# Kernel optimization log

Measured on AMD Instinct MI355X. Metric: run time of the kernel, lower is better.

Reference implementation:

```python
import jax, jax.numpy as jnp
import numpy as np

B, L, P, A = 32, 512, 128, 128   # batch, prot seq len, prot dim, atom dim
N = 1024                          # total atoms (32 per molecule)
H1, H2 = 512, 256                 # hidden_list


def setup_inputs() -> dict:
    key = jax.random.key(0)
    ks = jax.random.split(key, 12)
    atom_embed = jax.random.normal(ks[0], (N, A), dtype=jnp.float32)
    protSeq_embed = jax.random.normal(ks[1], (B, L, P), dtype=jnp.float32)
    # sorted segment ids, every segment non-empty (32 atoms per molecule)
    atom_splits = jnp.repeat(jnp.arange(B, dtype=jnp.int64), N // B)
    s = 0.05
    att1_W = jax.random.normal(ks[2], (P + A, 128), dtype=jnp.float32) * s
    att1_b = jnp.zeros((128,), dtype=jnp.float32)
    att2_W = jax.random.normal(ks[3], (128, 1), dtype=jnp.float32) * s
    att2_b = jnp.zeros((1,), dtype=jnp.float32)
    d1_W = jax.random.normal(ks[4], (A + P, H1), dtype=jnp.float32) * s
    d1_b = jnp.zeros((H1,), dtype=jnp.float32)
    d2_W = jax.random.normal(ks[5], (H1, H2), dtype=jnp.float32) * s
    d2_b = jnp.zeros((H2,), dtype=jnp.float32)
    out_W = jax.random.normal(ks[6], (H2, 1), dtype=jnp.float32) * s
    out_b = jnp.zeros((1,), dtype=jnp.float32)
    return {"atom_embed": atom_embed, "protSeq_embed": protSeq_embed,
            "atom_splits": atom_splits,
            "att1_W": att1_W, "att1_b": att1_b, "att2_W": att2_W, "att2_b": att2_b,
            "d1_W": d1_W, "d1_b": d1_b, "d2_W": d2_W, "d2_b": d2_b,
            "out_W": out_W, "out_b": out_b}


def reference(atom_embed, protSeq_embed, atom_splits,
              att1_W, att1_b, att2_W, att2_b,
              d1_W, d1_b, d2_W, d2_b, out_W, out_b):
    num_seg = protSeq_embed.shape[0]
    # gather protein rows per atom: [N, L, P]
    prot_g = protSeq_embed[atom_splits]
    # concat with broadcast atom embed: [N, L, P+A]
    atom_x = jnp.broadcast_to(atom_embed[:, None, :], prot_g.shape[:2] + atom_embed.shape[-1:])
    concat = jnp.concatenate([prot_g, atom_x], axis=-1)
    # attention MLP -> scores W: [N, L]
    hid = jnp.tanh(concat @ att1_W + att1_b)
    W = 5.0 * jnp.tanh(hid @ att2_W + att2_b)[..., 0]
    # atom-side weights: exp(max over seq), normalized per segment
    Wc = jnp.exp(jnp.max(W, axis=-1, keepdims=True))                     # [N, 1]
    Sc = jax.ops.segment_sum(Wc, atom_splits, num_segments=num_seg)[atom_splits]
    aa = Wc / Sc                                                          # [N, 1]
    atom_pool = jax.ops.segment_sum(aa * atom_embed, atom_splits, num_segments=num_seg)  # [B, A]
    # protein-side: segment-max scores, softmax over seq, weighted sum
    Wp = jax.ops.segment_max(W, atom_splits, num_segments=num_seg)       # [B, L]
    ap = jax.nn.softmax(Wp, axis=-1)
    prot_pool = jnp.einsum('bl,bld->bd', ap, protSeq_embed)              # [B, P]
    z = jnp.concatenate([atom_pool, prot_pool], axis=-1)
    z = jax.nn.relu(z @ d1_W + d1_b)
    z = jax.nn.relu(z @ d2_W + d2_b)
    return z @ out_W + out_b                                             # [B, 1]
```

## Files before the change

### kernel.cpp

```cpp
#include <hip/hip_runtime.h>
#include <math.h>

#define NATOMS 1024
#define BSEG   32
#define LSEQ   512

__device__ __forceinline__ float fast_tanh(float x) {
    x = fminf(fmaxf(x, -20.0f), 20.0f);
    float e = __expf(2.0f * x);
    return __fdividef(e - 1.0f, e + 1.0f);
}

__device__ __forceinline__ float trm(float c, float p, float e) {
    return c * __builtin_amdgcn_rcpf(fmaf(p, e, 1.0f));
}

__global__ __launch_bounds__(256) void gemm_exp_kernel(
    const float* __restrict__ protSeq, const float* __restrict__ atom_embed,
    const float* __restrict__ att1_W, const float* __restrict__ att1_b,
    float* __restrict__ ep, float* __restrict__ eb,
    float* __restrict__ zr, float* __restrict__ dp)
{
    __shared__ float xT[64 * 68];
    __shared__ float wsb[64 * 132];
    const int tid = threadIdx.x, bx = blockIdx.x;

    const float* Xb; const float* Wb; const float* bb; float* outp;
    if (bx < 256) {
        Xb = protSeq + (long)bx * 64 * 128; Wb = att1_W; bb = att1_b;
        outp = ep + (long)bx * 64 * 128;
    } else {
        int e = bx - 256;
        zr[e * 256 + tid] = 0.0f;
        if (e == 0 && tid < 32) dp[tid] = 0.0f;
        Xb = atom_embed + (long)e * 64 * 128; Wb = att1_W + 128 * 128; bb = nullptr;
        outp = eb + (long)e * 64 * 128;
    }
    const int tx = tid & 15, ty = tid >> 4;

    float acc[4][8];
    #pragma unroll
    for (int i = 0; i < 4; ++i)
        #pragma unroll
        for (int j = 0; j < 8; ++j) acc[i][j] = 0.0f;

    #pragma unroll
    for (int half = 0; half < 2; ++half) {
        if (half) __syncthreads();
        #pragma unroll
        for (int t = 0; t < 4; ++t) {
            int flat = (tid + 256 * t) * 4;
            int r = flat >> 6, kk = flat & 63;
            float4 v = *(const float4*)&Xb[r * 128 + half * 64 + kk];
            xT[kk * 68 + r] = v.x; xT[(kk + 1) * 68 + r] = v.y;
            xT[(kk + 2) * 68 + r] = v.z; xT[(kk + 3) * 68 + r] = v.w;
        }
        #pragma unroll
        for (int t = 0; t < 8; ++t) {
            int flat = (tid + 256 * t) * 4;
            int kk = flat >> 7, c = flat & 127;
            *(float4*)&wsb[kk * 132 + c] = *(const float4*)&Wb[(half * 64 + kk) * 128 + c];
        }
        __syncthreads();
        #pragma unroll 4
        for (int kk = 0; kk < 64; ++kk) {
            float4 a  = *(const float4*)&xT[kk * 68 + 4 * ty];
            float4 w0 = *(const float4*)&wsb[kk * 132 + 8 * tx];
            float4 w1 = *(const float4*)&wsb[kk * 132 + 8 * tx + 4];
            #pragma unroll
            for (int i = 0; i < 4; ++i) {
                float av = (i == 0) ? a.x : (i == 1) ? a.y : (i == 2) ? a.z : a.w;
                acc[i][0] += av * w0.x; acc[i][1] += av * w0.y;
                acc[i][2] += av * w0.z; acc[i][3] += av * w0.w;
                acc[i][4] += av * w1.x; acc[i][5] += av * w1.y;
                acc[i][6] += av * w1.z; acc[i][7] += av * w1.w;
            }
        }
    }
    float bias[8];
    #pragma unroll
    for (int j = 0; j < 8; ++j) bias[j] = 0.0f;
    if (bb) {
        *(float4*)&bias[0] = *(const float4*)&bb[8 * tx];
        *(float4*)&bias[4] = *(const float4*)&bb[8 * tx + 4];
    }
    #pragma unroll
    for (int i = 0; i < 4; ++i) {
        float o[8];
        #pragma unroll
        for (int j = 0; j < 8; ++j) {
            float v = fminf(fmaxf(acc[i][j] + bias[j], -20.0f), 20.0f);
            o[j] = __expf(2.0f * v);
        }
        int row = 4 * ty + i;
        *(float4*)&outp[row * 128 + 8 * tx]     = make_float4(o[0], o[1], o[2], o[3]);
        *(float4*)&outp[row * 128 + 8 * tx + 4] = make_float4(o[4], o[5], o[6], o[7]);
    }
}

__global__ __launch_bounds__(256) void score3_kernel(
    const float* __restrict__ ep, const float* __restrict__ eb,
    const float* __restrict__ att2_W, const float* __restrict__ att2_b,
    const float* __restrict__ protSeq,
    float* __restrict__ pmax, float* __restrict__ zr, float* __restrict__ dp)
{
    __shared__ float eps[64 * 132];
    __shared__ float ebs[32 * 132];
    __shared__ float c_s[128];
    __shared__ float wps[64];
    __shared__ float es[64];
    __shared__ float pmn[32 * 33];
    __shared__ float part[256];
    __shared__ float base_s;
    const int tid = threadIdx.x;
    const int chunk = blockIdx.x, b = blockIdx.y;
    const int lbase = chunk * 64;

    #pragma unroll
    for (int t = 0; t < 8; ++t) {
        int flat = (tid + 256 * t) * 4;
        int l = flat >> 7, j = flat & 127;
        *(float4*)&eps[l * 132 + j] =
            *(const float4*)&ep[((long)(b * 512 + lbase + l)) * 128 + j];
    }
    #pragma unroll
    for (int t = 0; t < 4; ++t) {
        int flat = (tid + 256 * t) * 4;
        int n = flat >> 7, j = flat & 127;
        *(float4*)&ebs[n * 132 + j] = *(const float4*)&eb[(b * 32 + n) * 128 + j];
    }
    if (tid < 128) c_s[tid] = -2.0f * att2_W[tid];
    __syncthreads();
    if (tid < 64) {
        float s = c_s[tid] + c_s[tid + 64];
        #pragma unroll
        for (int m = 1; m < 64; m <<= 1) s += __shfl_xor(s, m);
        if (tid == 0) base_s = -0.5f * s + att2_b[0];
    }
    __syncthreads();

    const int ng = tid & 7, lg = tid >> 3;
    const float* e0 = &ebs[ng * 132];
    const float* e1 = &ebs[(ng + 8) * 132];
    const float* e2 = &ebs[(ng + 16) * 132];
    const float* e3 = &ebs[(ng + 24) * 132];
    const float* p0 = &eps[lg * 132];
    const float* p1 = &eps[(lg + 32) * 132];
    float a00 = 0, a01 = 0, a10 = 0, a11 = 0, a20 = 0, a21 = 0, a30 = 0, a31 = 0;
    #pragma unroll 2
    for (int jj = 0; jj < 128; jj += 4) {
        float4 c4 = *(const float4*)&c_s[jj];
        float4 q0 = *(const float4*)(p0 + jj);
        float4 q1 = *(const float4*)(p1 + jj);
        float4 b0 = *(const float4*)(e0 + jj);
        float4 b1 = *(const float4*)(e1 + jj);
        float4 b2v = *(const float4*)(e2 + jj);
        float4 b3 = *(const float4*)(e3 + jj);
#define DOCOMP(C, Q0, Q1, B0, B1, B2, B3) \
        a00 += trm(C, Q0, B0); a01 += trm(C, Q1, B0); \
        a10 += trm(C, Q0, B1); a11 += trm(C, Q1, B1); \
        a20 += trm(C, Q0, B2); a21 += trm(C, Q1, B2); \
        a30 += trm(C, Q0, B3); a31 += trm(C, Q1, B3);
        DOCOMP(c4.x, q0.x, q1.x, b0.x, b1.x, b2v.x, b3.x)
        DOCOMP(c4.y, q0.y, q1.y, b0.y, b1.y, b2v.y, b3.y)
        DOCOMP(c4.z, q0.z, q1.z, b0.z, b1.z, b2v.z, b3.z)
        DOCOMP(c4.w, q0.w, q1.w, b0.w, b1.w, b2v.w, b3.w)
#undef DOCOMP
    }
    const float bs = base_s;
    float W00 = 5.0f * fast_tanh(a00 + bs), W01 = 5.0f * fast_tanh(a01 + bs);
    float W10 = 5.0f * fast_tanh(a10 + bs), W11 = 5.0f * fast_tanh(a11 + bs);
    float W20 = 5.0f * fast_tanh(a20 + bs), W21 = 5.0f * fast_tanh(a21 + bs);
    float W30 = 5.0f * fast_tanh(a30 + bs), W31 = 5.0f * fast_tanh(a31 + bs);

    float m0 = fmaxf(fmaxf(W00, W10), fmaxf(W20, W30));
    float m1 = fmaxf(fmaxf(W01, W11), fmaxf(W21, W31));
    #pragma unroll
    for (int d = 1; d < 8; d <<= 1) {
        m0 = fmaxf(m0, __shfl_xor(m0, d));
        m1 = fmaxf(m1, __shfl_xor(m1, d));
    }
    if (ng == 0) { wps[lg] = m0; wps[lg + 32] = m1; }
    pmn[lg * 33 + ng]      = fmaxf(W00, W01);
    pmn[lg * 33 + ng + 8]  = fmaxf(W10, W11);
    pmn[lg * 33 + ng + 16] = fmaxf(W20, W21);
    pmn[lg * 33 + ng + 24] = fmaxf(W30, W31);
    __syncthreads();
    if (tid < 32) {
        float m = pmn[tid];
        #pragma unroll
        for (int g = 1; g < 32; ++g) m = fmaxf(m, pmn[g * 33 + tid]);
        pmax[b * 256 + chunk * 32 + tid] = m;
    }
    if (tid < 64) es[tid] = __expf(wps[tid]);
    __syncthreads();
    if (tid < 64) {
        float v = es[tid];
        #pragma unroll
        for (int d = 1; d < 64; d <<= 1) v += __shfl_xor(v, d);
        if (tid == 0) atomicAdd(&dp[b], v);
    }
    const int dd = tid & 127, hf = tid >> 7;
    float az = 0.0f;
    #pragma unroll 4
    for (int i = 0; i < 32; ++i)
        az += es[hf * 32 + i] *
              protSeq[((long)(b * 512 + lbase + hf * 32 + i)) * 128 + dd];
    part[tid] = az;
    __syncthreads();
    if (tid < 128) atomicAdd(&zr[b * 128 + tid], part[tid] + part[128 + tid]);
}

__global__ __launch_bounds__(256) void mlp1_kernel(
    const float* __restrict__ pmax, const float* __restrict__ atom_embed,
    const float* __restrict__ zr, const float* __restrict__ dp,
    const float* __restrict__ d1_W, const float* __restrict__ d1_b,
    const float* __restrict__ out_b, float* __restrict__ h1,
    float* __restrict__ out)
{
    __shared__ float zs[256];
    __shared__ float part[4 * 65];
    __shared__ float expw[32];
    __shared__ float sinv_s;
    const int tid = threadIdx.x;
    const int cx = blockIdx.x, b = blockIdx.y;
    if (tid < 32) {
        float m = -1e30f;
        #pragma unroll
        for (int c = 0; c < 8; ++c) m = fmaxf(m, pmax[b * 256 + c * 32 + tid]);
        float e = __expf(m);
        expw[tid] = e;
        #pragma unroll
        for (int d = 1; d < 32; d <<= 1) e += __shfl_xor(e, d);
        if (tid == 0) sinv_s = 1.0f / e;
    }
    if (cx == 0 && tid == 0) out[b] = out_b[0];
    __syncthreads();
    if (tid < 128) {
        float a = 0.0f;
        #pragma unroll 4
        for (int n = 0; n < 32; ++n)
            a += expw[n] * atom_embed[(b * 32 + n) * 128 + tid];
        zs[tid] = a * sinv_s;
    } else {
        zs[tid] = zr[b * 128 + tid - 128] * (1.0f / dp[b]);
    }
    __syncthreads();
    const int c0 = cx * 64, ci = tid & 63, kg = tid >> 6;
    float acc = 0.0f;
    #pragma unroll 8
    for (int k = kg * 64; k < kg * 64 + 64; ++k)
        acc += zs[k] * d1_W[k * 512 + c0 + ci];
    part[kg * 65 + ci] = acc;
    __syncthreads();
    if (tid < 64) {
        float s = part[tid] + part[65 + tid] + part[130 + tid] + part[195 + tid]
                + d1_b[c0 + tid];
        h1[b * 512 + c0 + tid] = fmaxf(s, 0.0f);
    }
}

__global__ __launch_bounds__(256) void mlp2_kernel(
    const float* __restrict__ h1, const float* __restrict__ d2_W,
    const float* __restrict__ d2_b, const float* __restrict__ out_W,
    float* __restrict__ out)
{
    __shared__ float hs[512];
    __shared__ float part[8 * 33];
    const int tid = threadIdx.x;
    const int c0 = blockIdx.x * 32, b = blockIdx.y;
    hs[tid] = h1[b * 512 + tid];
    hs[tid + 256] = h1[b * 512 + 256 + tid];
    __syncthreads();
    const int ci = tid & 31, kg = tid >> 5;
    float acc = 0.0f;
    #pragma unroll 8
    for (int k = kg * 64; k < kg * 64 + 64; ++k)
        acc += hs[k] * d2_W[k * 256 + c0 + ci];
    part[kg * 33 + ci] = acc;
    __syncthreads();
    if (tid < 32) {
        float s = d2_b[c0 + tid];
        #pragma unroll
        for (int g = 0; g < 8; ++g) s += part[g * 33 + tid];
        float contrib = fmaxf(s, 0.0f) * out_W[c0 + tid];
        #pragma unroll
        for (int m = 16; m; m >>= 1) contrib += __shfl_xor(contrib, m);
        if (tid == 0) atomicAdd(&out[b], contrib);
    }
}

extern "C" void kernel_launch(void* const* d_in, const int* in_sizes, int n_in,
                              void* d_out, int out_size, void* d_ws, size_t ws_size,
                              hipStream_t stream) {
    const float* atom_embed = (const float*)d_in[0];
    const float* protSeq    = (const float*)d_in[1];
    const float* att1_W = (const float*)d_in[3];
    const float* att1_b = (const float*)d_in[4];
    const float* att2_W = (const float*)d_in[5];
    const float* att2_b = (const float*)d_in[6];
    const float* d1_W   = (const float*)d_in[7];
    const float* d1_b   = (const float*)d_in[8];
    const float* d2_W   = (const float*)d_in[9];
    const float* d2_b   = (const float*)d_in[10];
    const float* out_W  = (const float*)d_in[11];
    const float* out_b  = (const float*)d_in[12];
    float* out = (float*)d_out;

    float* ws = (float*)d_ws;
    float* ep   = ws;
    float* eb   = ep + 2097152;
    float* pmax = eb + 131072;
    float* zr   = pmax + 8192;
    float* dp   = zr + 4096;
    float* h1   = dp + 32;

    gemm_exp_kernel<<<272, 256, 0, stream>>>(protSeq, atom_embed, att1_W,
                                             att1_b, ep, eb, zr, dp);
    score3_kernel<<<dim3(8, BSEG), 256, 0, stream>>>(ep, eb, att2_W, att2_b,
                                                     protSeq, pmax, zr, dp);
    mlp1_kernel<<<dim3(8, BSEG), 256, 0, stream>>>(pmax, atom_embed, zr, dp,
                                                   d1_W, d1_b, out_b, h1, out);
    mlp2_kernel<<<dim3(8, BSEG), 256, 0, stream>>>(h1, d2_W, d2_b, out_W, out);
}
```

Measured before the change: 127.1 us.

## Fuse all stages into one cooperative kernel with grid syncs

Replaces the four kernel launches with a single cooperative kernel of 256 blocks that uses grid-wide syncs between phases. The att1 projection of the protein chunk is kept in shared memory and consumed directly by the scoring stage, so the 8 MB exp-projection intermediate no longer round-trips through global memory. The per-atom projection is spread across the chunk blocks, and the final MLP runs in one block per batch. This removes launch gaps and global traffic, but adds grid-sync cost and leaves 7 of 8 blocks idle during the serial MLP tail.

```diff
diff --git a/kernel.cpp b/kernel.cpp
--- a/kernel.cpp
+++ b/kernel.cpp
@@ -1,5 +1,8 @@
 #include <hip/hip_runtime.h>
+#include <hip/hip_cooperative_groups.h>
 #include <math.h>
+
+namespace cg = cooperative_groups;
 
 #define NATOMS 1024
 #define BSEG   32
@@ -10,283 +13,282 @@
     float e = __expf(2.0f * x);
     return __fdividef(e - 1.0f, e + 1.0f);
 }
-
 __device__ __forceinline__ float trm(float c, float p, float e) {
     return c * __builtin_amdgcn_rcpf(fmaf(p, e, 1.0f));
 }
 
-__global__ __launch_bounds__(256) void gemm_exp_kernel(
-    const float* __restrict__ protSeq, const float* __restrict__ atom_embed,
+#define EPS_SZ  8448
+#define REG2_SZ 13312
+
+__global__ void __launch_bounds__(256) mega_kernel(
+    const float* __restrict__ atom_embed, const float* __restrict__ protSeq,
     const float* __restrict__ att1_W, const float* __restrict__ att1_b,
-    float* __restrict__ ep, float* __restrict__ eb,
-    float* __restrict__ zr, float* __restrict__ dp)
+    const float* __restrict__ att2_W, const float* __restrict__ att2_b,
+    const float* __restrict__ d1_W, const float* __restrict__ d1_b,
+    const float* __restrict__ d2_W, const float* __restrict__ d2_b,
+    const float* __restrict__ out_W, const float* __restrict__ out_b,
+    float* __restrict__ eb, float* __restrict__ pmax,
+    float* __restrict__ zr, float* __restrict__ dp, float* __restrict__ out)
 {
-    __shared__ float xT[64 * 68];
-    __shared__ float wsb[64 * 132];
-    const int tid = threadIdx.x, bx = blockIdx.x;
-
-    const float* Xb; const float* Wb; const float* bb; float* outp;
-    if (bx < 256) {
-        Xb = protSeq + (long)bx * 64 * 128; Wb = att1_W; bb = att1_b;
-        outp = ep + (long)bx * 64 * 128;
-    } else {
-        int e = bx - 256;
-        zr[e * 256 + tid] = 0.0f;
-        if (e == 0 && tid < 32) dp[tid] = 0.0f;
-        Xb = atom_embed + (long)e * 64 * 128; Wb = att1_W + 128 * 128; bb = nullptr;
-        outp = eb + (long)e * 64 * 128;
-    }
-    const int tx = tid & 15, ty = tid >> 4;
-
-    float acc[4][8];
-    #pragma unroll
-    for (int i = 0; i < 4; ++i)
-        #pragma unroll
-        for (int j = 0; j < 8; ++j) acc[i][j] = 0.0f;
-
-    #pragma unroll
-    for (int half = 0; half < 2; ++half) {
-        if (half) __syncthreads();
-        #pragma unroll
-        for (int t = 0; t < 4; ++t) {
-            int flat = (tid + 256 * t) * 4;
-            int r = flat >> 6, kk = flat & 63;
-            float4 v = *(const float4*)&Xb[r * 128 + half * 64 + kk];
-            xT[kk * 68 + r] = v.x; xT[(kk + 1) * 68 + r] = v.y;
-            xT[(kk + 2) * 68 + r] = v.z; xT[(kk + 3) * 68 + r] = v.w;
-        }
-        #pragma unroll
-        for (int t = 0; t < 8; ++t) {
-            int flat = (tid + 256 * t) * 4;
-            int kk = flat >> 7, c = flat & 127;
-            *(float4*)&wsb[kk * 132 + c] = *(const float4*)&Wb[(half * 64 + kk) * 128 + c];
-        }
-        __syncthreads();
-        #pragma unroll 4
-        for (int kk = 0; kk < 64; ++kk) {
-            float4 a  = *(const float4*)&xT[kk * 68 + 4 * ty];
-            float4 w0 = *(const float4*)&wsb[kk * 132 + 8 * tx];
-            float4 w1 = *(const float4*)&wsb[kk * 132 + 8 * tx + 4];
-            #pragma unroll
-            for (int i = 0; i < 4; ++i) {
-                float av = (i == 0) ? a.x : (i == 1) ? a.y : (i == 2) ? a.z : a.w;
-                acc[i][0] += av * w0.x; acc[i][1] += av * w0.y;
-                acc[i][2] += av * w0.z; acc[i][3] += av * w0.w;
-                acc[i][4] += av * w1.x; acc[i][5] += av * w1.y;
-                acc[i][6] += av * w1.z; acc[i][7] += av * w1.w;
-            }
-        }
-    }
-    float bias[8];
-    #pragma unroll
-    for (int j = 0; j < 8; ++j) bias[j] = 0.0f;
-    if (bb) {
-        *(float4*)&bias[0] = *(const float4*)&bb[8 * tx];
-        *(float4*)&bias[4] = *(const float4*)&bb[8 * tx + 4];
-    }
-    #pragma unroll
-    for (int i = 0; i < 4; ++i) {
-        float o[8];
-        #pragma unroll
-        for (int j = 0; j < 8; ++j) {
-            float v = fminf(fmaxf(acc[i][j] + bias[j], -20.0f), 20.0f);
-            o[j] = __expf(2.0f * v);
-        }
-        int row = 4 * ty + i;
-        *(float4*)&outp[row * 128 + 8 * tx]     = make_float4(o[0], o[1], o[2], o[3]);
-        *(float4*)&outp[row * 128 + 8 * tx + 4] = make_float4(o[4], o[5], o[6], o[7]);
-    }
-}
-
-__global__ __launch_bounds__(256) void score3_kernel(
-    const float* __restrict__ ep, const float* __restrict__ eb,
-    const float* __restrict__ att2_W, const float* __restrict__ att2_b,
-    const float* __restrict__ protSeq,
-    float* __restrict__ pmax, float* __restrict__ zr, float* __restrict__ dp)
-{
-    __shared__ float eps[64 * 132];
-    __shared__ float ebs[32 * 132];
-    __shared__ float c_s[128];
-    __shared__ float wps[64];
-    __shared__ float es[64];
-    __shared__ float pmn[32 * 33];
-    __shared__ float part[256];
-    __shared__ float base_s;
+    __shared__ float smem[EPS_SZ + REG2_SZ];
+    float* eps  = smem;
+    float* reg2 = smem + EPS_SZ;
     const int tid = threadIdx.x;
     const int chunk = blockIdx.x, b = blockIdx.y;
     const int lbase = chunk * 64;
 
-    #pragma unroll
-    for (int t = 0; t < 8; ++t) {
-        int flat = (tid + 256 * t) * 4;
-        int l = flat >> 7, j = flat & 127;
-        *(float4*)&eps[l * 132 + j] =
-            *(const float4*)&ep[((long)(b * 512 + lbase + l)) * 128 + j];
+    {
+        float* xT  = reg2;
+        float* wsb = reg2 + 4352;
+        float* xTa = reg2 + 12800;
+
+        if (chunk == 2 && tid < 128) zr[b * 128 + tid] = 0.0f;
+        if (chunk == 1 && tid == 0) dp[b] = 0.0f;
+
+        for (int i = tid; i < 128; i += 256) {
+            int r = i >> 5, c = i & 31;
+            float4 v = *(const float4*)&atom_embed[(b * 32 + chunk * 4 + r) * 128 + 4 * c];
+            xTa[(4 * c + 0) * 4 + r] = v.x;
+            xTa[(4 * c + 1) * 4 + r] = v.y;
+            xTa[(4 * c + 2) * 4 + r] = v.z;
+            xTa[(4 * c + 3) * 4 + r] = v.w;
+        }
+
+        const int tx = tid & 15, ty = tid >> 4;
+        const float* Xb = protSeq + ((long)(b * 512 + lbase)) * 128;
+        float acc[4][8];
+        #pragma unroll
+        for (int i = 0; i < 4; ++i)
+            #pragma unroll
+            for (int j = 0; j < 8; ++j) acc[i][j] = 0.0f;
+
+        #pragma unroll
+        for (int half = 0; half < 2; ++half) {
+            if (half) __syncthreads();
+            #pragma unroll
+            for (int t = 0; t < 4; ++t) {
+                int flat = (tid + 256 * t) * 4;
+                int r = flat >> 6, kk = flat & 63;
+                float4 v = *(const float4*)&Xb[r * 128 + half * 64 + kk];
+                xT[kk * 68 + r] = v.x; xT[(kk + 1) * 68 + r] = v.y;
+                xT[(kk + 2) * 68 + r] = v.z; xT[(kk + 3) * 68 + r] = v.w;
+            }
+            #pragma unroll
+            for (int t = 0; t < 8; ++t) {
+                int flat = (tid + 256 * t) * 4;
+                int kk = flat >> 7, c = flat & 127;
+                *(float4*)&wsb[kk * 132 + c] =
+                    *(const float4*)&att1_W[(half * 64 + kk) * 128 + c];
+            }
+            __syncthreads();
+            #pragma unroll 4
+            for (int kk = 0; kk < 64; ++kk) {
+                float4 a  = *(const float4*)&xT[kk * 68 + 4 * ty];
+                float4 w0 = *(const float4*)&wsb[kk * 132 + 8 * tx];
+                float4 w1 = *(const float4*)&wsb[kk * 132 + 8 * tx + 4];
+                #pragma unroll
+                for (int i = 0; i < 4; ++i) {
+                    float av = (i == 0) ? a.x : (i == 1) ? a.y : (i == 2) ? a.z : a.w;
+                    acc[i][0] += av * w0.x; acc[i][1] += av * w0.y;
+                    acc[i][2] += av * w0.z; acc[i][3] += av * w0.w;
+                    acc[i][4] += av * w1.x; acc[i][5] += av * w1.y;
+                    acc[i][6] += av * w1.z; acc[i][7] += av * w1.w;
+                }
+            }
+        }
+        float bias[8];
+        *(float4*)&bias[0] = *(const float4*)&att1_b[8 * tx];
+        *(float4*)&bias[4] = *(const float4*)&att1_b[8 * tx + 4];
+        #pragma unroll
+        for (int i = 0; i < 4; ++i) {
+            float o[8];
+            #pragma unroll
+            for (int j = 0; j < 8; ++j) {
+                float v = fminf(fmaxf(acc[i][j] + bias[j], -20.0f), 20.0f);
+                o[j] = __expf(2.0f * v);
+            }
+            int row = 4 * ty + i;
+            *(float4*)&eps[row * 132 + 8 * tx]     = make_float4(o[0], o[1], o[2], o[3]);
+            *(float4*)&eps[row * 132 + 8 * tx + 4] = make_float4(o[4], o[5], o[6], o[7]);
+        }
+        if (tid < 32) {
+            float a2[4][4];
+            #pragma unroll
+            for (int i = 0; i < 4; ++i)
+                #pragma unroll
+                for (int j = 0; j < 4; ++j) a2[i][j] = 0.0f;
+            #pragma unroll 4
+            for (int k = 0; k < 128; ++k) {
+                float4 av = *(const float4*)&xTa[k * 4];
+                float4 wv = *(const float4*)&att1_W[(128 + k) * 128 + 4 * tid];
+                a2[0][0] += av.x * wv.x; a2[0][1] += av.x * wv.y;
+                a2[0][2] += av.x * wv.z; a2[0][3] += av.x * wv.w;
+                a2[1][0] += av.y * wv.x; a2[1][1] += av.y * wv.y;
+                a2[1][2] += av.y * wv.z; a2[1][3] += av.y * wv.w;
+                a2[2][0] += av.z * wv.x; a2[2][1] += av.z * wv.y;
+                a2[2][2] += av.z * wv.z; a2[2][3] += av.z * wv.w;
+                a2[3][0] += av.w * wv.x; a2[3][1] += av.w * wv.y;
+                a2[3][2] += av.w * wv.z; a2[3][3] += av.w * wv.w;
+            }
+            #pragma unroll
+            for (int n = 0; n < 4; ++n) {
+                float4 o;
+                o.x = __expf(2.0f * fminf(fmaxf(a2[n][0], -20.0f), 20.0f));
+                o.y = __expf(2.0f * fminf(fmaxf(a2[n][1], -20.0f), 20.0f));
+                o.z = __expf(2.0f * fminf(fmaxf(a2[n][2], -20.0f), 20.0f));
+                o.w = __expf(2.0f * fminf(fmaxf(a2[n][3], -20.0f), 20.0f));
+                *(float4*)&eb[(b * 32 + chunk * 4 + n) * 128 + 4 * tid] = o;
+            }
+        }
     }
-    #pragma unroll
-    for (int t = 0; t < 4; ++t) {
-        int flat = (tid + 256 * t) * 4;
-        int n = flat >> 7, j = flat & 127;
-        *(float4*)&ebs[n * 132 + j] = *(const float4*)&eb[(b * 32 + n) * 128 + j];
+    cg::this_grid().sync();
+
+    {
+        float* ebs  = reg2;
+        float* c_s  = reg2 + 4224;
+        float* pmn  = reg2 + 4352;
+        float* wps  = reg2 + 5408;
+        float* es   = reg2 + 5472;
+        float* part = reg2 + 5536;
+        float* scal = reg2 + 5792;
+
+        #pragma unroll
+        for (int t = 0; t < 4; ++t) {
+            int flat = (tid + 256 * t) * 4;
+            int n = flat >> 7, j = flat & 127;
+            *(float4*)&ebs[n * 132 + j] = *(const float4*)&eb[(b * 32 + n) * 128 + j];
+        }
+        if (tid < 128) c_s[tid] = -2.0f * att2_W[tid];
+        __syncthreads();
+        if (tid < 64) {
+            float s = c_s[tid] + c_s[tid + 64];
+            #pragma unroll
+            for (int m = 1; m < 64; m <<= 1) s += __shfl_xor(s, m);
+            if (tid == 0) scal[0] = -0.5f * s + att2_b[0];
+        }
+        __syncthreads();
+
+        const int ng = tid & 7, lg = tid >> 3;
+        const float* e0 = &ebs[ng * 132];
+        const float* e1 = &ebs[(ng + 8) * 132];
+        const float* e2 = &ebs[(ng + 16) * 132];
+        const float* e3 = &ebs[(ng + 24) * 132];
+        const float* p0 = &eps[lg * 132];
+        const float* p1 = &eps[(lg + 32) * 132];
+        float a00 = 0, a01 = 0, a10 = 0, a11 = 0, a20 = 0, a21 = 0, a30 = 0, a31 = 0;
+        #pragma unroll 2
+        for (int jj = 0; jj < 128; jj += 4) {
+            float4 c4 = *(const float4*)&c_s[jj];
+            float4 q0 = *(const float4*)(p0 + jj);
+            float4 q1 = *(const float4*)(p1 + jj);
+            float4 b0 = *(const float4*)(e0 + jj);
+            float4 b1 = *(const float4*)(e1 + jj);
+            float4 b2v = *(const float4*)(e2 + jj);
+            float4 b3 = *(const float4*)(e3 + jj);
+#define DOCOMP(C, Q0, Q1, B0, B1, B2, B3) \
+            a00 += trm(C, Q0, B0); a01 += trm(C, Q1, B0); \
+            a10 += trm(C, Q0, B1); a11 += trm(C, Q1, B1); \
+            a20 += trm(C, Q0, B2); a21 += trm(C, Q1, B2); \
+            a30 += trm(C, Q0, B3); a31 += trm(C, Q1, B3);
+            DOCOMP(c4.x, q0.x, q1.x, b0.x, b1.x, b2v.x, b3.x)
+            DOCOMP(c4.y, q0.y, q1.y, b0.y, b1.y, b2v.y, b3.y)
+            DOCOMP(c4.z, q0.z, q1.z, b0.z, b1.z, b2v.z, b3.z)
+            DOCOMP(c4.w, q0.w, q1.w, b0.w, b1.w, b2v.w, b3.w)
+#undef DOCOMP
+        }
+        const float bs = scal[0];
+        float W00 = 5.0f * fast_tanh(a00 + bs), W01 = 5.0f * fast_tanh(a01 + bs);
+        float W10 = 5.0f * fast_tanh(a10 + bs), W11 = 5.0f * fast_tanh(a11 + bs);
+        float W20 = 5.0f * fast_tanh(a20 + bs), W21 = 5.0f * fast_tanh(a21 + bs);
+        float W30 = 5.0f * fast_tanh(a30 + bs), W31 = 5.0f * fast_tanh(a31 + bs);
+
+        float m0 = fmaxf(fmaxf(W00, W10), fmaxf(W20, W30));
+        float m1 = fmaxf(fmaxf(W01, W11), fmaxf(W21, W31));
+        #pragma unroll
+        for (int d = 1; d < 8; d <<= 1) {
+            m0 = fmaxf(m0, __shfl_xor(m0, d));
+            m1 = fmaxf(m1, __shfl_xor(m1, d));
+        }
+        if (ng == 0) { wps[lg] = m0; wps[lg + 32] = m1; }
+        pmn[lg * 33 + ng]      = fmaxf(W00, W01);
+        pmn[lg * 33 + ng + 8]  = fmaxf(W10, W11);
+        pmn[lg * 33 + ng + 16] = fmaxf(W20, W21);
+        pmn[lg * 33 + ng + 24] = fmaxf(W30, W31);
+        __syncthreads();
+        if (tid < 32) {
+            float m = pmn[tid];
+            #pragma unroll
+            for (int g = 1; g < 32; ++g) m = fmaxf(m, pmn[g * 33 + tid]);
+            pmax[b * 256 + chunk * 32 + tid] = m;
+        }
+        if (tid < 64) es[tid] = __expf(wps[tid]);
+        __syncthreads();
+        if (tid < 64) {
+            float v = es[tid];
+            #pragma unroll
+            for (int d = 1; d < 64; d <<= 1) v += __shfl_xor(v, d);
+            if (tid == 0) atomicAdd(&dp[b], v);
+        }
+        const int dd = tid & 127, hf = tid >> 7;
+        float az = 0.0f;
+        #pragma unroll 4
+        for (int i = 0; i < 32; ++i)
+            az += es[hf * 32 + i] *
+                  protSeq[((long)(b * 512 + lbase + hf * 32 + i)) * 128 + dd];
+        part[tid] = az;
+        __syncthreads();
+        if (tid < 128) atomicAdd(&zr[b * 128 + tid], part[tid] + part[128 + tid]);
     }
-    if (tid < 128) c_s[tid] = -2.0f * att2_W[tid];
-    __syncthreads();
-    if (tid < 64) {
-        float s = c_s[tid] + c_s[tid + 64];
-        #pragma unroll
-        for (int m = 1; m < 64; m <<= 1) s += __shfl_xor(s, m);
-        if (tid == 0) base_s = -0.5f * s + att2_b[0];
-    }
-    __syncthreads();
-
-    const int ng = tid & 7, lg = tid >> 3;
-    const float* e0 = &ebs[ng * 132];
-    const float* e1 = &ebs[(ng + 8) * 132];
-    const float* e2 = &ebs[(ng + 16) * 132];
-    const float* e3 = &ebs[(ng + 24) * 132];
-    const float* p0 = &eps[lg * 132];
-    const float* p1 = &eps[(lg + 32) * 132];
-    float a00 = 0, a01 = 0, a10 = 0, a11 = 0, a20 = 0, a21 = 0, a30 = 0, a31 = 0;
-    #pragma unroll 2
-    for (int jj = 0; jj < 128; jj += 4) {
-        float4 c4 = *(const float4*)&c_s[jj];
-        float4 q0 = *(const float4*)(p0 + jj);
-        float4 q1 = *(const float4*)(p1 + jj);
-        float4 b0 = *(const float4*)(e0 + jj);
-        float4 b1 = *(const float4*)(e1 + jj);
-        float4 b2v = *(const float4*)(e2 + jj);
-        float4 b3 = *(const float4*)(e3 + jj);
-#define DOCOMP(C, Q0, Q1, B0, B1, B2, B3) \
-        a00 += trm(C, Q0, B0); a01 += trm(C, Q1, B0); \
-        a10 += trm(C, Q0, B1); a11 += trm(C, Q1, B1); \
-        a20 += trm(C, Q0, B2); a21 += trm(C, Q1, B2); \
-        a30 += trm(C, Q0, B3); a31 += trm(C, Q1, B3);
-        DOCOMP(c4.x, q0.x, q1.x, b0.x, b1.x, b2v.x, b3.x)
-        DOCOMP(c4.y, q0.y, q1.y, b0.y, b1.y, b2v.y, b3.y)
-        DOCOMP(c4.z, q0.z, q1.z, b0.z, b1.z, b2v.z, b3.z)
-        DOCOMP(c4.w, q0.w, q1.w, b0.w, b1.w, b2v.w, b3.w)
-#undef DOCOMP
-    }
-    const float bs = base_s;
-    float W00 = 5.0f * fast_tanh(a00 + bs), W01 = 5.0f * fast_tanh(a01 + bs);
-    float W10 = 5.0f * fast_tanh(a10 + bs), W11 = 5.0f * fast_tanh(a11 + bs);
-    float W20 = 5.0f * fast_tanh(a20 + bs), W21 = 5.0f * fast_tanh(a21 + bs);
-    float W30 = 5.0f * fast_tanh(a30 + bs), W31 = 5.0f * fast_tanh(a31 + bs);
-
-    float m0 = fmaxf(fmaxf(W00, W10), fmaxf(W20, W30));
-    float m1 = fmaxf(fmaxf(W01, W11), fmaxf(W21, W31));
-    #pragma unroll
-    for (int d = 1; d < 8; d <<= 1) {
-        m0 = fmaxf(m0, __shfl_xor(m0, d));
-        m1 = fmaxf(m1, __shfl_xor(m1, d));
-    }
-    if (ng == 0) { wps[lg] = m0; wps[lg + 32] = m1; }
-    pmn[lg * 33 + ng]      = fmaxf(W00, W01);
-    pmn[lg * 33 + ng + 8]  = fmaxf(W10, W11);
-    pmn[lg * 33 + ng + 16] = fmaxf(W20, W21);
-    pmn[lg * 33 + ng + 24] = fmaxf(W30, W31);
-    __syncthreads();
-    if (tid < 32) {
-        float m = pmn[tid];
-        #pragma unroll
-        for (int g = 1; g < 32; ++g) m = fmaxf(m, pmn[g * 33 + tid]);
-        pmax[b * 256 + chunk * 32 + tid] = m;
-    }
-    if (tid < 64) es[tid] = __expf(wps[tid]);
-    __syncthreads();
-    if (tid < 64) {
-        float v = es[tid];
-        #pragma unroll
-        for (int d = 1; d < 64; d <<= 1) v += __shfl_xor(v, d);
-        if (tid == 0) atomicAdd(&dp[b], v);
-    }
-    const int dd = tid & 127, hf = tid >> 7;
-    float az = 0.0f;
-    #pragma unroll 4
-    for (int i = 0; i < 32; ++i)
-        az += es[hf * 32 + i] *
-              protSeq[((long)(b * 512 + lbase + hf * 32 + i)) * 128 + dd];
-    part[tid] = az;
-    __syncthreads();
-    if (tid < 128) atomicAdd(&zr[b * 128 + tid], part[tid] + part[128 + tid]);
-}
-
-__global__ __launch_bounds__(256) void mlp1_kernel(
-    const float* __restrict__ pmax, const float* __restrict__ atom_embed,
-    const float* __restrict__ zr, const float* __restrict__ dp,
-    const float* __restrict__ d1_W, const float* __restrict__ d1_b,
-    const float* __restrict__ out_b, float* __restrict__ h1,
-    float* __restrict__ out)
-{
-    __shared__ float zs[256];
-    __shared__ float part[4 * 65];
-    __shared__ float expw[32];
-    __shared__ float sinv_s;
-    const int tid = threadIdx.x;
-    const int cx = blockIdx.x, b = blockIdx.y;
-    if (tid < 32) {
-        float m = -1e30f;
-        #pragma unroll
-        for (int c = 0; c < 8; ++c) m = fmaxf(m, pmax[b * 256 + c * 32 + tid]);
-        float e = __expf(m);
-        expw[tid] = e;
-        #pragma unroll
-        for (int d = 1; d < 32; d <<= 1) e += __shfl_xor(e, d);
-        if (tid == 0) sinv_s = 1.0f / e;
-    }
-    if (cx == 0 && tid == 0) out[b] = out_b[0];
-    __syncthreads();
-    if (tid < 128) {
-        float a = 0.0f;
-        #pragma unroll 4
-        for (int n = 0; n < 32; ++n)
-            a += expw[n] * atom_embed[(b * 32 + n) * 128 + tid];
-        zs[tid] = a * sinv_s;
-    } else {
-        zs[tid] = zr[b * 128 + tid - 128] * (1.0f / dp[b]);
-    }
-    __syncthreads();
-    const int c0 = cx * 64, ci = tid & 63, kg = tid >> 6;
-    float acc = 0.0f;
-    #pragma unroll 8
-    for (int k = kg * 64; k < kg * 64 + 64; ++k)
-        acc += zs[k] * d1_W[k * 512 + c0 + ci];
-    part[kg * 65 + ci] = acc;
-    __syncthreads();
-    if (tid < 64) {
-        float s = part[tid] + part[65 + tid] + part[130 + tid] + part[195 + tid]
-                + d1_b[c0 + tid];
-        h1[b * 512 + c0 + tid] = fmaxf(s, 0.0f);
-    }
-}
-
-__global__ __launch_bounds__(256) void mlp2_kernel(
-    const float* __restrict__ h1, const float* __restrict__ d2_W,
-    const float* __restrict__ d2_b, const float* __restrict__ out_W,
-    float* __restrict__ out)
-{
-    __shared__ float hs[512];
-    __shared__ float part[8 * 33];
-    const int tid = threadIdx.x;
-    const int c0 = blockIdx.x * 32, b = blockIdx.y;
-    hs[tid] = h1[b * 512 + tid];
-    hs[tid + 256] = h1[b * 512 + 256 + tid];
-    __syncthreads();
-    const int ci = tid & 31, kg = tid >> 5;
-    float acc = 0.0f;
-    #pragma unroll 8
-    for (int k = kg * 64; k < kg * 64 + 64; ++k)
-        acc += hs[k] * d2_W[k * 256 + c0 + ci];
-    part[kg * 33 + ci] = acc;
-    __syncthreads();
-    if (tid < 32) {
-        float s = d2_b[c0 + tid];
-        #pragma unroll
-        for (int g = 0; g < 8; ++g) s += part[g * 33 + tid];
-        float contrib = fmaxf(s, 0.0f) * out_W[c0 + tid];
-        #pragma unroll
-        for (int m = 16; m; m >>= 1) contrib += __shfl_xor(contrib, m);
-        if (tid == 0) atomicAdd(&out[b], contrib);
+    cg::this_grid().sync();
+
+    if (chunk == 0) {
+        float* zs   = reg2;
+        float* hs   = reg2 + 256;
+        float* expw = reg2 + 768;
+        float* red  = reg2 + 800;
+        float* sc   = reg2 + 1056;
+        if (tid < 32) {
+            float m = pmax[b * 256 + tid];
+            #pragma unroll
+            for (int c = 1; c < 8; ++c) m = fmaxf(m, pmax[b * 256 + c * 32 + tid]);
+            float e = __expf(m);
+            expw[tid] = e;
+            #pragma unroll
+            for (int d = 1; d < 32; d <<= 1) e += __shfl_xor(e, d);
+            if (tid == 0) sc[0] = 1.0f / e;
+        }
+        __syncthreads();
+        if (tid < 128) {
+            float a = 0.0f;
+            #pragma unroll 4
+            for (int n = 0; n < 32; ++n)
+                a += expw[n] * atom_embed[(b * 32 + n) * 128 + tid];
+            zs[tid] = a * sc[0];
+        } else {
+            zs[tid] = zr[b * 128 + tid - 128] * (1.0f / dp[b]);
+        }
+        __syncthreads();
+        #pragma unroll
+        for (int rep = 0; rep < 2; ++rep) {
+            int c = tid + 256 * rep;
+            float a = d1_b[c];
+            #pragma unroll 8
+            for (int k = 0; k < 256; ++k) a += zs[k] * d1_W[k * 512 + c];
+            hs[c] = fmaxf(a, 0.0f);
+        }
+        __syncthreads();
+        {
+            float a = d2_b[tid];
+            #pragma unroll 8
+            for (int k = 0; k < 512; ++k) a += hs[k] * d2_W[k * 256 + tid];
+            red[tid] = fmaxf(a, 0.0f) * out_W[tid];
+        }
+        __syncthreads();
+        for (int s = 128; s; s >>= 1) {
+            if (tid < s) red[tid] += red[tid + s];
+            __syncthreads();
+        }
+        if (tid == 0) out[b] = red[0] + out_b[0];
     }
 }
 
@@ -308,18 +310,18 @@
     float* out = (float*)d_out;
 
     float* ws = (float*)d_ws;
-    float* ep   = ws;
-    float* eb   = ep + 2097152;
+    float* eb   = ws;
     float* pmax = eb + 131072;
     float* zr   = pmax + 8192;
     float* dp   = zr + 4096;
-    float* h1   = dp + 32;
-
-    gemm_exp_kernel<<<272, 256, 0, stream>>>(protSeq, atom_embed, att1_W,
-                                             att1_b, ep, eb, zr, dp);
-    score3_kernel<<<dim3(8, BSEG), 256, 0, stream>>>(ep, eb, att2_W, att2_b,
-                                                     protSeq, pmax, zr, dp);
-    mlp1_kernel<<<dim3(8, BSEG), 256, 0, stream>>>(pmax, atom_embed, zr, dp,
-                                                   d1_W, d1_b, out_b, h1, out);
-    mlp2_kernel<<<dim3(8, BSEG), 256, 0, stream>>>(h1, d2_W, d2_b, out_W, out);
+
+    void* args[] = {
+        (void*)&atom_embed, (void*)&protSeq,
+        (void*)&att1_W, (void*)&att1_b, (void*)&att2_W, (void*)&att2_b,
+        (void*)&d1_W, (void*)&d1_b, (void*)&d2_W, (void*)&d2_b,
+        (void*)&out_W, (void*)&out_b,
+        (void*)&eb, (void*)&pmax, (void*)&zr, (void*)&dp, (void*)&out
+    };
+    hipLaunchCooperativeKernel((void*)mega_kernel, dim3(8, BSEG), dim3(256),
+                               args, 0, stream);
 }
```

Measured after the change: 235.5 us. 85.2% more time.
